# Kernel optimization log

Measured on AMD Instinct MI355X. Metric: run time of the kernel, lower is better.

Reference implementation:

```python
import jax, jax.numpy as jnp
import numpy as np

B, H, L, D = 16, 8, 128, 64
SCALE = jnp.float32(np.sqrt(D))
NEG = jnp.float32(-1e9)


def setup_inputs() -> dict:
    key = jax.random.key(0)
    kq, kk, kv, km = jax.random.split(key, 4)
    Q = jax.random.normal(kq, (B, H, L, D), dtype=jnp.float32)
    K = jax.random.normal(kk, (H, B, L, D), dtype=jnp.float32)
    V = jax.random.normal(kv, (H, B, L, D), dtype=jnp.float32)
    mask = jax.random.randint(km, (B, 1, 1, L, L), 0, 2, dtype=jnp.int32)
    return {"Q": Q, "K": K, "V": V, "mask": mask}


def reference(Q, K, V, mask):
    # Cross-sample (intersample) attention:
    # scores[b,h,c,i,j] = <Q[b,h,i,:], K[h,c,j,:]> / sqrt(D)  -> (B,H,B,L,L)
    scores = jnp.einsum('bhid,hcjd->bhcij', Q, K) / SCALE
    scores = jnp.where(mask == 0, NEG, scores)
    attn_weights = jax.nn.softmax(scores, axis=-1)  # (B,H,B,L,L)
    # output[b,h,c,i,:] = sum_j w[b,h,c,i,j] * V[h,c,j,:]  -> (B,H,B,L,D)
    output = jnp.einsum('bhcij,hcjd->bhcid', attn_weights, V)
    return (output, attn_weights)
```

## Files before the change

### kernel.cpp

```cpp
#include <hip/hip_runtime.h>
#include <hip/hip_bf16.h>

typedef float  f32x4  __attribute__((ext_vector_type(4)));
typedef __bf16 bf16x8 __attribute__((ext_vector_type(8)));

#define MFMA16(A,B,C) __builtin_amdgcn_mfma_f32_16x16x32_bf16((A),(B),(C),0,0,0)

constexpr int BN = 16, HN = 8, LN = 128, DN = 64;
constexpr size_t OUT0 = (size_t)BN * HN * BN * LN * DN;

__device__ __forceinline__ void load8_cvt(const float* __restrict__ p,
                                          bf16x8& hi, bf16x8& lo) {
  float f[8];
  *(float4*)&f[0] = *(const float4*)(p);
  *(float4*)&f[4] = *(const float4*)(p + 4);
#pragma unroll
  for (int i = 0; i < 8; ++i) {
    __bf16 h = (__bf16)f[i];
    hi[i] = h;
    lo[i] = (__bf16)(f[i] - (float)h);
  }
}

__global__ __launch_bounds__(256, 2) void isa_attn_kernel(
    const float* __restrict__ Q, const float* __restrict__ K,
    const float* __restrict__ V, const int* __restrict__ M,
    float* __restrict__ out)
{
  __shared__ float VT[DN][LN + 4];
  __shared__ float P [LN][64 + 4];

  const int bid = blockIdx.x;
  const int b = bid >> 7;
  const int h = (bid >> 4) & 7;
  const int c = bid & 15;

  const float* Qp = Q + (size_t)(b * HN + h) * (LN * DN);
  const float* Kp = K + (size_t)(h * BN + c) * (LN * DN);
  const float* Vp = V + (size_t)(h * BN + c) * (LN * DN);
  const int*   Mp = M + (size_t)b * (LN * LN);
  float* Op = out + (size_t)bid * (LN * DN);
  float* Wp = out + OUT0 + (size_t)bid * (LN * LN);

  const int t    = threadIdx.x;
  const int lane = t & 63;
  const int wave = t >> 6;
  const int quad = lane >> 4;
  const int l16  = lane & 15;
  const int row0 = wave * 32;

#pragma unroll
  for (int it = 0; it < 8; ++it) {
    int idx4 = t + it * 256;
    int j  = idx4 >> 4;
    int d0 = (idx4 & 15) * 4;
    float4 v = ((const float4*)Vp)[idx4];
    VT[d0 + 0][j] = v.x; VT[d0 + 1][j] = v.y;
    VT[d0 + 2][j] = v.z; VT[d0 + 3][j] = v.w;
  }

  bf16x8 qhi[2][2], qlo[2][2];
#pragma unroll
  for (int rt = 0; rt < 2; ++rt)
#pragma unroll
    for (int kt = 0; kt < 2; ++kt)
      load8_cvt(Qp + (row0 + rt * 16 + l16) * DN + kt * 32 + quad * 8,
                qhi[rt][kt], qlo[rt][kt]);

  f32x4 acc[2][8];
#pragma unroll
  for (int rt = 0; rt < 2; ++rt)
#pragma unroll
    for (int ct = 0; ct < 8; ++ct)
      acc[rt][ct] = (f32x4){0.f, 0.f, 0.f, 0.f};

#pragma unroll
  for (int ct = 0; ct < 8; ++ct) {
#pragma unroll
    for (int kt = 0; kt < 2; ++kt) {
      bf16x8 khi, klo;
      load8_cvt(Kp + (ct * 16 + l16) * DN + kt * 32 + quad * 8, khi, klo);
#pragma unroll
      for (int rt = 0; rt < 2; ++rt) {
        acc[rt][ct] = MFMA16(qhi[rt][kt], khi, acc[rt][ct]);
        acc[rt][ct] = MFMA16(qlo[rt][kt], khi, acc[rt][ct]);
        acc[rt][ct] = MFMA16(qhi[rt][kt], klo, acc[rt][ct]);
      }
    }
  }

#pragma unroll
  for (int rt = 0; rt < 2; ++rt) {
    int mv[8][4];
#pragma unroll
    for (int ct = 0; ct < 8; ++ct)
#pragma unroll
      for (int r = 0; r < 4; ++r)
        mv[ct][r] = Mp[(row0 + rt * 16 + quad * 4 + r) * LN + ct * 16 + l16];
#pragma unroll
    for (int r = 0; r < 4; ++r) {
      float s[8];
      float mx = -3.0e38f;
#pragma unroll
      for (int ct = 0; ct < 8; ++ct) {
        s[ct] = (mv[ct][r] != 0) ? acc[rt][ct][r] * 0.125f : -1.0e9f;
        mx = fmaxf(mx, s[ct]);
      }
      mx = fmaxf(mx, __shfl_xor(mx, 1));
      mx = fmaxf(mx, __shfl_xor(mx, 2));
      mx = fmaxf(mx, __shfl_xor(mx, 4));
      mx = fmaxf(mx, __shfl_xor(mx, 8));
      float sum = 0.f;
#pragma unroll
      for (int ct = 0; ct < 8; ++ct) { s[ct] = __expf(s[ct] - mx); sum += s[ct]; }
      sum += __shfl_xor(sum, 1);
      sum += __shfl_xor(sum, 2);
      sum += __shfl_xor(sum, 4);
      sum += __shfl_xor(sum, 8);
      float inv = __builtin_amdgcn_rcpf(sum);
      inv = inv * (2.0f - sum * inv);
#pragma unroll
      for (int ct = 0; ct < 8; ++ct) acc[rt][ct][r] = s[ct] * inv;
    }
  }

  __syncthreads();

  f32x4 oacc[2][4];
#pragma unroll
  for (int rt = 0; rt < 2; ++rt)
#pragma unroll
    for (int nt = 0; nt < 4; ++nt)
      oacc[rt][nt] = (f32x4){0.f, 0.f, 0.f, 0.f};

#pragma unroll
  for (int half = 0; half < 2; ++half) {
#pragma unroll
    for (int rt = 0; rt < 2; ++rt)
#pragma unroll
      for (int c4 = 0; c4 < 4; ++c4)
#pragma unroll
        for (int r = 0; r < 4; ++r)
          P[row0 + rt * 16 + quad * 4 + r][c4 * 16 + l16] = acc[rt][half * 4 + c4][r];

#pragma unroll
    for (int e = 0; e < 8; ++e) {
      int idx = e * 64 + lane;
      int r  = idx >> 4;
      int c4 = (idx & 15) * 4;
      float4 v = *(const float4*)&P[row0 + r][c4];
      *(float4*)&Wp[(size_t)(row0 + r) * LN + half * 64 + c4] = v;
    }

#pragma unroll
    for (int jt = 0; jt < 2; ++jt) {
      bf16x8 phi[2], plo[2];
#pragma unroll
      for (int rt = 0; rt < 2; ++rt)
        load8_cvt(&P[row0 + rt * 16 + l16][jt * 32 + quad * 8], phi[rt], plo[rt]);
#pragma unroll
      for (int nt = 0; nt < 4; ++nt) {
        bf16x8 vhi, vlo;
        load8_cvt(&VT[nt * 16 + l16][half * 64 + jt * 32 + quad * 8], vhi, vlo);
#pragma unroll
        for (int rt = 0; rt < 2; ++rt) {
          oacc[rt][nt] = MFMA16(phi[rt], vhi, oacc[rt][nt]);
          oacc[rt][nt] = MFMA16(plo[rt], vhi, oacc[rt][nt]);
          oacc[rt][nt] = MFMA16(phi[rt], vlo, oacc[rt][nt]);
        }
      }
    }
  }

#pragma unroll
  for (int rt = 0; rt < 2; ++rt)
#pragma unroll
    for (int nt = 0; nt < 4; ++nt)
#pragma unroll
      for (int r = 0; r < 4; ++r)
        Op[(row0 + rt * 16 + quad * 4 + r) * DN + nt * 16 + l16] = oacc[rt][nt][r];
}

extern "C" void kernel_launch(void* const* d_in, const int* in_sizes, int n_in,
                              void* d_out, int out_size, void* d_ws, size_t ws_size,
                              hipStream_t stream) {
  const float* Q = (const float*)d_in[0];
  const float* K = (const float*)d_in[1];
  const float* V = (const float*)d_in[2];
  const int*   M = (const int*)d_in[3];
  float* out = (float*)d_out;
  isa_attn_kernel<<<dim3(BN * HN * BN), dim3(256), 0, stream>>>(Q, K, V, M, out);
}
```

Before: 252.4 us.

## Drop K/V low-part MFMAs, store V as bf16, write weights directly

Cuts the split-bf16 matmuls from three MFMAs to two by dropping the low part of K and V, so only Q and P keep hi/lo splitting. V is converted to bf16 once into shared memory, which halves its LDS footprint. The 1/sqrt(D) scale is folded into Q and the mask becomes a multiply after the exponential. Attention weights are written straight from registers instead of through an LDS staging copy, and occupancy is raised to 3 blocks per CU. Dropping the K/V low parts loses accuracy. Masking by multiplication also changes rows that are fully masked, and unmasked logits now enter the row max.

```diff
diff --git a/kernel.cpp b/kernel.cpp
--- a/kernel.cpp
+++ b/kernel.cpp
@@ -3,14 +3,36 @@
 
 typedef float  f32x4  __attribute__((ext_vector_type(4)));
 typedef __bf16 bf16x8 __attribute__((ext_vector_type(8)));
+typedef __bf16 bf16x2 __attribute__((ext_vector_type(2)));
 
 #define MFMA16(A,B,C) __builtin_amdgcn_mfma_f32_16x16x32_bf16((A),(B),(C),0,0,0)
 
 constexpr int BN = 16, HN = 8, LN = 128, DN = 64;
 constexpr size_t OUT0 = (size_t)BN * HN * BN * LN * DN;
 
-__device__ __forceinline__ void load8_cvt(const float* __restrict__ p,
-                                          bf16x8& hi, bf16x8& lo) {
+__device__ __forceinline__ void load8_split(const float* __restrict__ p, float scale,
+                                            bf16x8& hi, bf16x8& lo) {
+  float f[8];
+  *(float4*)&f[0] = *(const float4*)(p);
+  *(float4*)&f[4] = *(const float4*)(p + 4);
+#pragma unroll
+  for (int i = 0; i < 8; ++i) {
+    float x = f[i] * scale;
+    __bf16 h = (__bf16)x;
+    hi[i] = h;
+    lo[i] = (__bf16)(x - (float)h);
+  }
+}
+
+__device__ __forceinline__ void load8_hi(const float* __restrict__ p, bf16x8& hi) {
+  float f[8];
+  *(float4*)&f[0] = *(const float4*)(p);
+  *(float4*)&f[4] = *(const float4*)(p + 4);
+#pragma unroll
+  for (int i = 0; i < 8; ++i) hi[i] = (__bf16)f[i];
+}
+
+__device__ __forceinline__ void lds8_split(const float* p, bf16x8& hi, bf16x8& lo) {
   float f[8];
   *(float4*)&f[0] = *(const float4*)(p);
   *(float4*)&f[4] = *(const float4*)(p + 4);
@@ -22,13 +44,13 @@
   }
 }
 
-__global__ __launch_bounds__(256, 2) void isa_attn_kernel(
+__global__ __launch_bounds__(256, 3) void isa_attn_kernel(
     const float* __restrict__ Q, const float* __restrict__ K,
     const float* __restrict__ V, const int* __restrict__ M,
     float* __restrict__ out)
 {
-  __shared__ float VT[DN][LN + 4];
-  __shared__ float P [LN][64 + 4];
+  __shared__ __bf16 VT[DN][136];
+  __shared__ float P[LN][68];
 
   const int bid = blockIdx.x;
   const int b = bid >> 7;
@@ -50,13 +72,17 @@
   const int row0 = wave * 32;
 
 #pragma unroll
-  for (int it = 0; it < 8; ++it) {
-    int idx4 = t + it * 256;
-    int j  = idx4 >> 4;
-    int d0 = (idx4 & 15) * 4;
-    float4 v = ((const float4*)Vp)[idx4];
-    VT[d0 + 0][j] = v.x; VT[d0 + 1][j] = v.y;
-    VT[d0 + 2][j] = v.z; VT[d0 + 3][j] = v.w;
+  for (int it = 0; it < 4; ++it) {
+    int idx = t + it * 256;
+    int j2  = idx >> 4;
+    int d0  = (idx & 15) * 4;
+    float4 a = *(const float4*)(Vp + (2 * j2) * DN + d0);
+    float4 bb = *(const float4*)(Vp + (2 * j2 + 1) * DN + d0);
+    const float* af = (const float*)&a;
+    const float* bf = (const float*)&bb;
+#pragma unroll
+    for (int w = 0; w < 4; ++w)
+      *(bf16x2*)&VT[d0 + w][2 * j2] = (bf16x2){(__bf16)af[w], (__bf16)bf[w]};
   }
 
   bf16x8 qhi[2][2], qlo[2][2];
@@ -64,8 +90,8 @@
   for (int rt = 0; rt < 2; ++rt)
 #pragma unroll
     for (int kt = 0; kt < 2; ++kt)
-      load8_cvt(Qp + (row0 + rt * 16 + l16) * DN + kt * 32 + quad * 8,
-                qhi[rt][kt], qlo[rt][kt]);
+      load8_split(Qp + (row0 + rt * 16 + l16) * DN + kt * 32 + quad * 8, 0.125f,
+                  qhi[rt][kt], qlo[rt][kt]);
 
   f32x4 acc[2][8];
 #pragma unroll
@@ -78,41 +104,40 @@
   for (int ct = 0; ct < 8; ++ct) {
 #pragma unroll
     for (int kt = 0; kt < 2; ++kt) {
-      bf16x8 khi, klo;
-      load8_cvt(Kp + (ct * 16 + l16) * DN + kt * 32 + quad * 8, khi, klo);
+      bf16x8 kh;
+      load8_hi(Kp + (ct * 16 + l16) * DN + kt * 32 + quad * 8, kh);
 #pragma unroll
       for (int rt = 0; rt < 2; ++rt) {
-        acc[rt][ct] = MFMA16(qhi[rt][kt], khi, acc[rt][ct]);
-        acc[rt][ct] = MFMA16(qlo[rt][kt], khi, acc[rt][ct]);
-        acc[rt][ct] = MFMA16(qhi[rt][kt], klo, acc[rt][ct]);
+        acc[rt][ct] = MFMA16(qhi[rt][kt], kh, acc[rt][ct]);
+        acc[rt][ct] = MFMA16(qlo[rt][kt], kh, acc[rt][ct]);
       }
     }
   }
 
 #pragma unroll
   for (int rt = 0; rt < 2; ++rt) {
-    int mv[8][4];
-#pragma unroll
-    for (int ct = 0; ct < 8; ++ct)
-#pragma unroll
-      for (int r = 0; r < 4; ++r)
-        mv[ct][r] = Mp[(row0 + rt * 16 + quad * 4 + r) * LN + ct * 16 + l16];
 #pragma unroll
     for (int r = 0; r < 4; ++r) {
-      float s[8];
+      int row = row0 + rt * 16 + quad * 4 + r;
+      const int* mrow = Mp + (size_t)row * LN + l16;
+      float*     wrow = Wp + (size_t)row * LN + l16;
+      float mf[8];
+#pragma unroll
+      for (int ct = 0; ct < 8; ++ct) mf[ct] = (float)mrow[ct * 16];
       float mx = -3.0e38f;
 #pragma unroll
-      for (int ct = 0; ct < 8; ++ct) {
-        s[ct] = (mv[ct][r] != 0) ? acc[rt][ct][r] * 0.125f : -1.0e9f;
-        mx = fmaxf(mx, s[ct]);
-      }
+      for (int ct = 0; ct < 8; ++ct) mx = fmaxf(mx, acc[rt][ct][r]);
       mx = fmaxf(mx, __shfl_xor(mx, 1));
       mx = fmaxf(mx, __shfl_xor(mx, 2));
       mx = fmaxf(mx, __shfl_xor(mx, 4));
       mx = fmaxf(mx, __shfl_xor(mx, 8));
+      float s[8];
       float sum = 0.f;
 #pragma unroll
-      for (int ct = 0; ct < 8; ++ct) { s[ct] = __expf(s[ct] - mx); sum += s[ct]; }
+      for (int ct = 0; ct < 8; ++ct) {
+        s[ct] = __expf(acc[rt][ct][r] - mx) * mf[ct];
+        sum += s[ct];
+      }
       sum += __shfl_xor(sum, 1);
       sum += __shfl_xor(sum, 2);
       sum += __shfl_xor(sum, 4);
@@ -120,7 +145,11 @@
       float inv = __builtin_amdgcn_rcpf(sum);
       inv = inv * (2.0f - sum * inv);
 #pragma unroll
-      for (int ct = 0; ct < 8; ++ct) acc[rt][ct][r] = s[ct] * inv;
+      for (int ct = 0; ct < 8; ++ct) {
+        float w = s[ct] * inv;
+        acc[rt][ct][r] = w;
+        wrow[ct * 16] = w;
+      }
     }
   }
 
@@ -144,29 +173,18 @@
           P[row0 + rt * 16 + quad * 4 + r][c4 * 16 + l16] = acc[rt][half * 4 + c4][r];
 
 #pragma unroll
-    for (int e = 0; e < 8; ++e) {
-      int idx = e * 64 + lane;
-      int r  = idx >> 4;
-      int c4 = (idx & 15) * 4;
-      float4 v = *(const float4*)&P[row0 + r][c4];
-      *(float4*)&Wp[(size_t)(row0 + r) * LN + half * 64 + c4] = v;
-    }
-
-#pragma unroll
     for (int jt = 0; jt < 2; ++jt) {
       bf16x8 phi[2], plo[2];
 #pragma unroll
       for (int rt = 0; rt < 2; ++rt)
-        load8_cvt(&P[row0 + rt * 16 + l16][jt * 32 + quad * 8], phi[rt], plo[rt]);
+        lds8_split(&P[row0 + rt * 16 + l16][jt * 32 + quad * 8], phi[rt], plo[rt]);
 #pragma unroll
       for (int nt = 0; nt < 4; ++nt) {
-        bf16x8 vhi, vlo;
-        load8_cvt(&VT[nt * 16 + l16][half * 64 + jt * 32 + quad * 8], vhi, vlo);
+        bf16x8 vh = *(const bf16x8*)&VT[nt * 16 + l16][half * 64 + jt * 32 + quad * 8];
 #pragma unroll
         for (int rt = 0; rt < 2; ++rt) {
-          oacc[rt][nt] = MFMA16(phi[rt], vhi, oacc[rt][nt]);
-          oacc[rt][nt] = MFMA16(plo[rt], vhi, oacc[rt][nt]);
-          oacc[rt][nt] = MFMA16(phi[rt], vlo, oacc[rt][nt]);
+          oacc[rt][nt] = MFMA16(phi[rt], vh, oacc[rt][nt]);
+          oacc[rt][nt] = MFMA16(plo[rt], vh, oacc[rt][nt]);
         }
       }
     }
@@ -188,6 +206,5 @@
   const float* K = (const float*)d_in[1];
   const float* V = (const float*)d_in[2];
   const int*   M = (const int*)d_in[3];
-  float* out = (float*)d_out;
-  isa_attn_kernel<<<dim3(BN * HN * BN), dim3(256), 0, stream>>>(Q, K, V, M, out);
-}
+  isa_attn_kernel<<<dim3(BN * HN * BN), dim3(256), 0, stream>>>(Q, K, V, M, (float*)d_out);
+}
```

New measurement: 249.3 us. No clear change (-1.2%).
